# Kernel optimization log

Hardware: AMD Instinct MI355X
Metric: run time of the kernel (lower is better)

## Reference

```python
import jax, jax.numpy as jnp
import numpy as np

B, T, C, H = 2, 2048, 1024, 16
D = C // H  # head dim = 64


def setup_inputs() -> dict:
    key = jax.random.key(0)
    k1, k2, k3 = jax.random.split(key, 3)
    x = jax.random.normal(k1, (B, T, C), dtype=jnp.float32)
    w_attn = jax.random.normal(k2, (C, 3 * C), dtype=jnp.float32) * (1.0 / np.sqrt(C))
    b_attn = jnp.zeros((3 * C,), dtype=jnp.float32)
    w_proj = jax.random.normal(k3, (C, C), dtype=jnp.float32) * (1.0 / np.sqrt(C))
    b_proj = jnp.zeros((C,), dtype=jnp.float32)
    return {"x": x, "w_attn": w_attn, "b_attn": b_attn, "w_proj": w_proj, "b_proj": b_proj}


def reference(x, w_attn, b_attn, w_proj, b_proj):
    Bx, Tx, Cx = x.shape
    qkv = x @ w_attn + b_attn  # [B, T, 3C]
    q, k, v = jnp.split(qkv, 3, axis=-1)
    # [B, H, T, D]
    q = q.reshape(Bx, Tx, H, D).swapaxes(1, 2)
    k = k.reshape(Bx, Tx, H, D).swapaxes(1, 2)
    v = v.reshape(Bx, Tx, H, D).swapaxes(1, 2)
    scale = 1.0 / jnp.sqrt(jnp.float32(D))
    att = jnp.einsum('bhqd,bhkd->bhqk', q, k) * scale  # [B, H, T, T]
    causal = jnp.tril(jnp.ones((Tx, Tx), dtype=bool))
    att = jnp.where(causal[None, None], att, -jnp.inf)
    att = jax.nn.softmax(att, axis=-1)
    y = jnp.einsum('bhqk,bhkd->bhqd', att, v)  # [B, H, T, D]
    y = y.swapaxes(1, 2).reshape(Bx, Tx, Cx)
    return y @ w_proj + b_proj
```

## Files before the change

### kernel.cpp

```cpp
#include <hip/hip_runtime.h>
#include <hip/hip_bf16.h>


typedef __attribute__((ext_vector_type(8))) short short8x;
typedef __attribute__((ext_vector_type(4))) float float4x;
typedef __attribute__((ext_vector_type(4))) unsigned short ushort4x;
typedef __attribute__((ext_vector_type(2))) unsigned int uint2x;

#define MFMA_BF16 __builtin_amdgcn_mfma_f32_16x16x32_bf16

typedef const __attribute__((address_space(1))) void gvoid_t;
typedef __attribute__((address_space(3))) void lvoid_t;
#define GLOAD_LDS16(g, l) __builtin_amdgcn_global_load_lds((gvoid_t*)(g), (lvoid_t*)(l), 16, 0, 0)

__device__ __forceinline__ unsigned short f2b(float f) {
    unsigned int u = __float_as_uint(f);
    u = (u + 0x7FFFu + ((u >> 16) & 1u)) >> 16;
    return (unsigned short)u;
}
__device__ __forceinline__ unsigned int pk2(float a, float b) {
    return __builtin_amdgcn_perm(__float_as_uint(b) + 0x8000u,
                                 __float_as_uint(a) + 0x8000u, 0x07060302u);
}

__device__ __forceinline__ void stage32(const unsigned short* g, size_t rs,
                                        short* ldst, int w0, int lane) {
    const int r8 = lane >> 3;
    const int sc = ((lane & 7) ^ r8) * 8;
#pragma unroll
    for (int q = 0; q < 4; q++) {
        GLOAD_LDS16(g + (size_t)(w0 + q * 8 + r8) * rs + sc,
                    ldst + (w0 + q * 8) * 64);
    }
}

__global__ __launch_bounds__(256) void cast_bf16(const float* __restrict__ in,
                                                 unsigned short* __restrict__ out,
                                                 int n4) {
    int i = blockIdx.x * 256 + threadIdx.x;
    if (i < n4) {
        float4 v = ((const float4*)in)[i];
        ushort4x o = { f2b(v.x), f2b(v.y), f2b(v.z), f2b(v.w) };
        ((ushort4x*)out)[i] = o;
    }
}

__global__ __launch_bounds__(256) void transpose_cast2(const float* __restrict__ wa,
                                                       unsigned short* __restrict__ waT,
                                                       const float* __restrict__ wp,
                                                       unsigned short* __restrict__ wpT) {
    __shared__ float tile[32][33];
    int bx = blockIdx.x;
    const float* in;
    unsigned short* outp;
    int cols;
    if (bx < 96) { in = wa; outp = waT; cols = 3072; }
    else         { in = wp; outp = wpT; cols = 1024; bx -= 96; }
    int cbase = bx * 32;
    int rbase = blockIdx.y * 32;
    int c = cbase + threadIdx.x;
    for (int j = 0; j < 32; j += 8)
        tile[threadIdx.y + j][threadIdx.x] = in[(size_t)(rbase + threadIdx.y + j) * cols + c];
    __syncthreads();
    int rr = rbase + threadIdx.x;
    for (int j = 0; j < 32; j += 8) {
        int cc = cbase + threadIdx.y + j;
        outp[(size_t)cc * 1024 + rr] = f2b(tile[threadIdx.x][threadIdx.y + j]);
    }
}

__global__ __launch_bounds__(256) void gemm_qkv(const unsigned short* __restrict__ A,
                                                const unsigned short* __restrict__ BT,
                                                const float* __restrict__ bias,
                                                unsigned short* __restrict__ QK,
                                                unsigned short* __restrict__ VTg) {
    __shared__ union {
        struct { short A[128 * 64]; short B[128 * 64]; } s;
        short vt[4][64 * 80];
    } lds;

    const int K = 1024;
    const int lane = threadIdx.x & 63;
    const int wave = threadIdx.x >> 6;
    const int quad = lane >> 4;
    const int l16  = lane & 15;
    const int sw   = l16 & 7;

    const int rblk = blockIdx.y * 128;
    const int cblk = blockIdx.x * 128;
    const int wr = wave >> 1, wc = wave & 1;

    float4x acc[4][4] = {};

    const unsigned short* Ag = A  + (size_t)rblk * K;
    const unsigned short* Bg = BT + (size_t)cblk * K;

    for (int kk = 0; kk < K; kk += 64) {
        stage32(Ag + kk, K, lds.s.A, wave * 32, lane);
        stage32(Bg + kk, K, lds.s.B, wave * 32, lane);
        __syncthreads();

#pragma unroll
        for (int kk2 = 0; kk2 < 2; kk2++) {
            short8x a[4], b[4];
#pragma unroll
            for (int i = 0; i < 4; i++)
                a[i] = *(const short8x*)&lds.s.A[(wr * 64 + i * 16 + l16) * 64 +
                                                 ((kk2 * 4 + quad) ^ sw) * 8];
#pragma unroll
            for (int j = 0; j < 4; j++)
                b[j] = *(const short8x*)&lds.s.B[(wc * 64 + j * 16 + l16) * 64 +
                                                 ((kk2 * 4 + quad) ^ sw) * 8];
#pragma unroll
            for (int i = 0; i < 4; i++)
#pragma unroll
                for (int j = 0; j < 4; j++)
                    acc[i][j] = MFMA_BF16(a[i], b[j], acc[i][j], 0, 0, 0);
        }
        __syncthreads();
    }

    const int rbase = rblk + wr * 64;
    const int cbase = cblk + wc * 64;

    if (cbase < 2048) {
        const float QS = 0.18033688f;
#pragma unroll
        for (int i = 0; i < 4; i++) {
#pragma unroll
            for (int j = 0; j < 4; j++) {
                int c = cbase + j * 16 + l16;
                float bv = bias[c];
                float sc = (c < 1024) ? QS : 1.0f;
#pragma unroll
                for (int reg = 0; reg < 4; reg++) {
                    int r = rbase + i * 16 + quad * 4 + reg;
                    QK[(size_t)r * 2048 + c] = f2b((acc[i][j][reg] + bv) * sc);
                }
            }
        }
    } else {
#pragma unroll
        for (int i = 0; i < 4; i++) {
#pragma unroll
            for (int j = 0; j < 4; j++) {
                int c = cbase + j * 16 + l16;
                float bv = bias[c];
                uint2x p = { pk2(acc[i][j][0] + bv, acc[i][j][1] + bv),
                             pk2(acc[i][j][2] + bv, acc[i][j][3] + bv) };
                *(uint2x*)&lds.vt[wave][(j * 16 + l16) * 80 + i * 16 + quad * 4] = p;
            }
        }
        const int h   = (cbase - 2048) >> 6;
        const int hb  = (rbase >> 11) * 16 + h;
        const int tb0 = rbase & 2047;
#pragma unroll
        for (int p = 0; p < 8; p++) {
            int dd   = p * 8 + (lane >> 3);
            int toff = (lane & 7) * 8;
            short8x vv = *(const short8x*)&lds.vt[wave][dd * 80 + toff];
            *(short8x*)&VTg[((size_t)(hb * 64 + dd)) * 2048 + tb0 + toff] = vv;
        }
    }
}

__global__ __launch_bounds__(256) void gemm_proj(const unsigned short* __restrict__ A,
                                                 const unsigned short* __restrict__ BT,
                                                 const float* __restrict__ bias,
                                                 float* __restrict__ out) {
    __shared__ struct { short A[64 * 64]; short B[64 * 64]; } lds;

    const int K = 1024, N = 1024;
    const int lane = threadIdx.x & 63;
    const int wave = threadIdx.x >> 6;
    const int quad = lane >> 4;
    const int l16  = lane & 15;
    const int sw   = l16 & 7;

    const int rblk = blockIdx.y * 64;
    const int cblk = blockIdx.x * 64;

    float4x acc[4] = {};

    const unsigned short* Ag = A  + (size_t)rblk * K;
    const unsigned short* Bg = BT + (size_t)cblk * K;

    for (int kk = 0; kk < K; kk += 64) {
        if (wave < 2) stage32(Ag + kk, K, lds.A, wave * 32, lane);
        else          stage32(Bg + kk, K, lds.B, (wave - 2) * 32, lane);
        __syncthreads();

#pragma unroll
        for (int kk2 = 0; kk2 < 2; kk2++) {
            short8x bfr = *(const short8x*)&lds.B[(wave * 16 + l16) * 64 +
                                                  ((kk2 * 4 + quad) ^ sw) * 8];
#pragma unroll
            for (int i = 0; i < 4; i++) {
                short8x a = *(const short8x*)&lds.A[(i * 16 + l16) * 64 +
                                                    ((kk2 * 4 + quad) ^ sw) * 8];
                acc[i] = MFMA_BF16(a, bfr, acc[i], 0, 0, 0);
            }
        }
        __syncthreads();
    }

    const int c = cblk + wave * 16 + l16;
    const float bv = bias[c];
#pragma unroll
    for (int i = 0; i < 4; i++) {
#pragma unroll
        for (int reg = 0; reg < 4; reg++) {
            int r = rblk + i * 16 + quad * 4 + reg;
            out[(size_t)r * N + c] = acc[i][reg] + bv;
        }
    }
}

__global__ __launch_bounds__(256) void attn_kernel(const unsigned short* __restrict__ QK,
                                                   const unsigned short* __restrict__ VT,
                                                   unsigned short* __restrict__ Y) {
    __shared__ __attribute__((aligned(16))) short Kl[2][64 * 64];
    __shared__ __attribute__((aligned(16))) short Vl[2][64 * 64];
    __shared__ __attribute__((aligned(16))) short Pl[4][16 * 64];

    const int tid  = threadIdx.x;
    const int lane = tid & 63;
    const int wave = tid >> 6;
    const int quad = lane >> 4;
    const int l16  = lane & 15;
    const int sw   = l16 & 7;

    const int bid = blockIdx.x;
    const int v2  = (bid >> 8) & 3;
    const int s2  = ((bid >> 3) & 3) ^ v2;
    const int m3  = (bid >> 5) & 7;
    const int qb  = (s2 == 0) ? m3 : (s2 == 1) ? 15 - m3
                  : (s2 == 2) ? 16 + m3 : 31 - m3;
    const int bh  = (bid & 7) | (v2 << 3);
    const int b = bh >> 4, h = bh & 15;

    const unsigned short* Qp = QK + ((size_t)b * 2048) * 2048 + h * 64;
    const unsigned short* Kp = Qp + 1024;
    const unsigned short* Vp = VT + (size_t)bh * 64 * 2048;

    const int qbase = qb * 64 + wave * 16;
    const int ntb   = qb + 1;

    short8x aq[2];
#pragma unroll
    for (int kk = 0; kk < 2; kk++)
        aq[kk] = *(const short8x*)(Qp + (size_t)(qbase + l16) * 2048 + kk * 32 + quad * 8);

    if (wave < 2) stage32(Kp, 2048, Kl[0], wave * 32, lane);
    else          stage32(Vp, 2048, Vl[0], (wave - 2) * 32, lane);
    __syncthreads();

    float l = 0.f;
    float4x O[4] = {};

    for (int it = 0; it < ntb; it++) {
        const int kb = it * 64;
        const short* Kc = Kl[it & 1];
        const short* Vc = Vl[it & 1];

        if (it + 1 < ntb) {
            const int kb2 = kb + 64;
            if (wave < 2) stage32(Kp + (size_t)kb2 * 2048, 2048, Kl[(it + 1) & 1], wave * 32, lane);
            else          stage32(Vp + kb2, 2048, Vl[(it + 1) & 1], (wave - 2) * 32, lane);
        }

        float4x S[4];
#pragma unroll
        for (int t = 0; t < 4; t++) {
            short8x kf0 = *(const short8x*)&Kc[(t * 16 + l16) * 64 + ((quad) ^ sw) * 8];
            short8x kf1 = *(const short8x*)&Kc[(t * 16 + l16) * 64 + ((4 + quad) ^ sw) * 8];
            S[t] = (float4x){0.f, 0.f, 0.f, 0.f};
            S[t] = MFMA_BF16(kf0, aq[0], S[t], 0, 0, 0);
            S[t] = MFMA_BF16(kf1, aq[1], S[t], 0, 0, 0);
        }

        if (kb + 64 > qbase) {
            int q = qbase + l16;
#pragma unroll
            for (int t = 0; t < 4; t++)
#pragma unroll
                for (int reg = 0; reg < 4; reg++)
                    if (kb + t * 16 + quad * 4 + reg > q) S[t][reg] = -1e38f;
        }

#pragma unroll
        for (int t = 0; t < 4; t++) {
            float e0 = __builtin_amdgcn_exp2f(S[t][0]);
            float e1 = __builtin_amdgcn_exp2f(S[t][1]);
            float e2 = __builtin_amdgcn_exp2f(S[t][2]);
            float e3 = __builtin_amdgcn_exp2f(S[t][3]);
            l += (e0 + e1) + (e2 + e3);
            uint2x p = { pk2(e0, e1), pk2(e2, e3) };
            *(uint2x*)&Pl[wave][l16 * 64 + ((2 * t + (quad >> 1)) ^ sw) * 8 + (quad & 1) * 4] = p;
        }

#pragma unroll
        for (int kc = 0; kc < 2; kc++) {
            short8x bp = *(const short8x*)&Pl[wave][l16 * 64 + ((4 * kc + quad) ^ sw) * 8];
#pragma unroll
            for (int dt = 0; dt < 4; dt++) {
                short8x vf = *(const short8x*)&Vc[(dt * 16 + l16) * 64 + ((kc * 4 + quad) ^ sw) * 8];
                O[dt] = MFMA_BF16(vf, bp, O[dt], 0, 0, 0);
            }
        }
        __syncthreads();
    }

    float lv = l;
    lv += __shfl_xor(lv, 16, 64);
    lv += __shfl_xor(lv, 32, 64);
    float rl = 1.0f / lv;
#pragma unroll
    for (int dt = 0; dt < 4; dt++) {
        uint2x o = { pk2(O[dt][0] * rl, O[dt][1] * rl),
                     pk2(O[dt][2] * rl, O[dt][3] * rl) };
        *(uint2x*)&Pl[wave][l16 * 64 + ((2 * dt + (quad >> 1)) ^ sw) * 8 + (quad & 1) * 4] = o;
    }
    const int t = qbase + l16;
#pragma unroll
    for (int cc = 0; cc < 2; cc++) {
        short8x row = *(const short8x*)&Pl[wave][l16 * 64 + ((2 * quad + cc) ^ sw) * 8];
        *(short8x*)&Y[((size_t)(b * 2048 + t)) * 1024 + h * 64 + (2 * quad + cc) * 8] = row;
    }
}

extern "C" void kernel_launch(void* const* d_in, const int* in_sizes, int n_in,
                              void* d_out, int out_size, void* d_ws, size_t ws_size,
                              hipStream_t stream) {
    const float* x      = (const float*)d_in[0];
    const float* w_attn = (const float*)d_in[1];
    const float* b_attn = (const float*)d_in[2];
    const float* w_proj = (const float*)d_in[3];
    const float* b_proj = (const float*)d_in[4];
    float* out = (float*)d_out;

    char* ws = (char*)d_ws;
    unsigned short* xb  = (unsigned short*)(ws + (size_t)0);
    unsigned short* waT = (unsigned short*)(ws + (size_t)(8  << 20));
    unsigned short* wpT = (unsigned short*)(ws + (size_t)(14 << 20));
    unsigned short* QKb = (unsigned short*)(ws + (size_t)(16 << 20));
    unsigned short* VTb = (unsigned short*)(ws + (size_t)(32 << 20));
    unsigned short* yb  = (unsigned short*)(ws + (size_t)(40 << 20));

    cast_bf16<<<4096, 256, 0, stream>>>(x, xb, 1048576);

    transpose_cast2<<<dim3(128, 32), dim3(32, 8), 0, stream>>>(w_attn, waT, w_proj, wpT);

    gemm_qkv<<<dim3(24, 32), 256, 0, stream>>>(xb, waT, b_attn, QKb, VTb);

    attn_kernel<<<1024, 256, 0, stream>>>(QKb, VTb, yb);

    gemm_proj<<<dim3(16, 64), 256, 0, stream>>>(yb, wpT, b_proj, out);
}
```

Baseline: 182.3 us.

## Double-buffer LDS staging in QKV and projection GEMMs, vectorize Q/K stores

Both GEMMs now prefetch the next K-slice into a second LDS buffer while computing on the current one, so global-to-LDS loads overlap MFMA work. The QKV GEMM moves to 32-wide K tiles with a new swizzle so the doubled buffers fit in the same LDS footprint. For Q/K tiles it swaps the MFMA operands so each lane holds four consecutive columns, which allows packed 8-byte bf16 stores and float4 bias loads. This adds per-iteration branching and changes the synchronisation pattern; the loop tail in the new code is not fully visible.

```diff
diff --git a/kernel.cpp b/kernel.cpp
--- a/kernel.cpp
+++ b/kernel.cpp
@@ -31,6 +31,17 @@
     for (int q = 0; q < 4; q++) {
         GLOAD_LDS16(g + (size_t)(w0 + q * 8 + r8) * rs + sc,
                     ldst + (w0 + q * 8) * 64);
+    }
+}
+
+__device__ __forceinline__ void stage32k32(const unsigned short* g, size_t rs,
+                                           short* ldst, int w0, int lane) {
+    const int r4 = lane >> 2;
+    const int sc = ((lane & 3) ^ ((lane >> 3) & 3)) * 8;
+#pragma unroll
+    for (int q = 0; q < 2; q++) {
+        GLOAD_LDS16(g + (size_t)(w0 + q * 16 + r4) * rs + sc,
+                    ldst + (w0 + q * 16) * 32);
     }
 }
 
@@ -75,7 +86,7 @@
                                                 unsigned short* __restrict__ QK,
                                                 unsigned short* __restrict__ VTg) {
     __shared__ union {
-        struct { short A[128 * 64]; short B[128 * 64]; } s;
+        struct { short A[2][128 * 32]; short B[2][128 * 32]; } s;
         short vt[4][64 * 80];
     } lds;
 
@@ -84,33 +95,43 @@
     const int wave = threadIdx.x >> 6;
     const int quad = lane >> 4;
     const int l16  = lane & 15;
-    const int sw   = l16 & 7;
+    const int co   = (quad ^ ((l16 >> 1) & 3)) * 8;
 
     const int rblk = blockIdx.y * 128;
     const int cblk = blockIdx.x * 128;
     const int wr = wave >> 1, wc = wave & 1;
+    const bool qk = (blockIdx.x < 16);
 
     float4x acc[4][4] = {};
 
     const unsigned short* Ag = A  + (size_t)rblk * K;
     const unsigned short* Bg = BT + (size_t)cblk * K;
 
-    for (int kk = 0; kk < K; kk += 64) {
-        stage32(Ag + kk, K, lds.s.A, wave * 32, lane);
-        stage32(Bg + kk, K, lds.s.B, wave * 32, lane);
-        __syncthreads();
-
-#pragma unroll
-        for (int kk2 = 0; kk2 < 2; kk2++) {
-            short8x a[4], b[4];
+    stage32k32(Ag, K, lds.s.A[0], wave * 32, lane);
+    stage32k32(Bg, K, lds.s.B[0], wave * 32, lane);
+    __syncthreads();
+
+    for (int it = 0; it < 32; ++it) {
+        const short* As = lds.s.A[it & 1];
+        const short* Bs = lds.s.B[it & 1];
+        if (it + 1 < 32) {
+            stage32k32(Ag + (it + 1) * 32, K, lds.s.A[(it + 1) & 1], wave * 32, lane);
+            stage32k32(Bg + (it + 1) * 32, K, lds.s.B[(it + 1) & 1], wave * 32, lane);
+        }
+        short8x a[4], b[4];
+#pragma unroll
+        for (int i = 0; i < 4; i++)
+            a[i] = *(const short8x*)&As[(wr * 64 + i * 16 + l16) * 32 + co];
+#pragma unroll
+        for (int j = 0; j < 4; j++)
+            b[j] = *(const short8x*)&Bs[(wc * 64 + j * 16 + l16) * 32 + co];
+        if (qk) {
 #pragma unroll
             for (int i = 0; i < 4; i++)
-                a[i] = *(const short8x*)&lds.s.A[(wr * 64 + i * 16 + l16) * 64 +
-                                                 ((kk2 * 4 + quad) ^ sw) * 8];
-#pragma unroll
-            for (int j = 0; j < 4; j++)
-                b[j] = *(const short8x*)&lds.s.B[(wc * 64 + j * 16 + l16) * 64 +
-                                                 ((kk2 * 4 + quad) ^ sw) * 8];
+#pragma unroll
+                for (int j = 0; j < 4; j++)
+                    acc[i][j] = MFMA_BF16(b[j], a[i], acc[i][j], 0, 0, 0);
+        } else {
 #pragma unroll
             for (int i = 0; i < 4; i++)
 #pragma unroll
@@ -123,20 +144,18 @@
     const int rbase = rblk + wr * 64;
     const int cbase = cblk + wc * 64;
 
-    if (cbase < 2048) {
-        const float QS = 0.18033688f;
+    if (qk) {
+        const float sc = (blockIdx.x < 8) ? 0.18033688f : 1.0f;
 #pragma unroll
         for (int i = 0; i < 4; i++) {
+            const int r = rbase + i * 16 + l16;
 #pragma unroll
             for (int j = 0; j < 4; j++) {
-                int c = cbase + j * 16 + l16;
-                float bv = bias[c];
-                float sc = (c < 1024) ? QS : 1.0f;
-#pragma unroll
-                for (int reg = 0; reg < 4; reg++) {
-                    int r = rbase + i * 16 + quad * 4 + reg;
-                    QK[(size_t)r * 2048 + c] = f2b((acc[i][j][reg] + bv) * sc);
-                }
+                const int c = cbase + j * 16 + quad * 4;
+                float4 bv = *(const float4*)&bias[c];
+                uint2x p = { pk2((acc[i][j][0] + bv.x) * sc, (acc[i][j][1] + bv.y) * sc),
+                             pk2((acc[i][j][2] + bv.z) * sc, (acc[i][j][3] + bv.w) * sc) };
+                *(uint2x*)&QK[(size_t)r * 2048 + c] = p;
             }
         }
     } else {
@@ -168,7 +187,7 @@
                                                  const unsigned short* __restrict__ BT,
                                                  const float* __restrict__ bias,
                                                  float* __restrict__ out) {
-    __shared__ struct { short A[64 * 64]; short B[64 * 64]; } lds;
+    __shared__ struct { short A[2][64 * 64]; short B[2][64 * 64]; } lds;
 
     const int K = 1024, N = 1024;
     const int lane = threadIdx.x & 63;
@@ -185,19 +204,26 @@
     const unsigned short* Ag = A  + (size_t)rblk * K;
     const unsigned short* Bg = BT + (size_t)cblk * K;
 
-    for (int kk = 0; kk < K; kk += 64) {
-        if (wave < 2) stage32(Ag + kk, K, lds.A, wave * 32, lane);
-        else          stage32(Bg + kk, K, lds.B, (wave - 2) * 32, lane);
-        __syncthreads();
-
+    if (wave < 2) stage32(Ag, K, lds.A[0], wave * 32, lane);
+    else          stage32(Bg, K, lds.B[0], (wave - 2) * 32, lane);
+    __syncthreads();
+
+    for (int it = 0; it < 16; ++it) {
+        const short* As = lds.A[it & 1];
+        const short* Bs = lds.B[it & 1];
+        if (it + 1 < 16) {
+            const int kk = (it + 1) * 64;
+            if (wave < 2) stage32(Ag + kk, K, lds.A[(it + 1) & 1], wave * 32, lane);
+            else          stage32(Bg + kk, K, lds.B[(it + 1) & 1], (wave - 2) * 32, lane);
+        }
 #pragma unroll
         for (int kk2 = 0; kk2 < 2; kk2++) {
-            short8x bfr = *(const short8x*)&lds.B[(wave * 16 + l16) * 64 +
-                                                  ((kk2 * 4 + quad) ^ sw) * 8];
+            short8x bfr = *(const short8x*)&Bs[(wave * 16 + l16) * 64 +
+                                               ((kk2 * 4 + quad) ^ sw) * 8];
 #pragma unroll
             for (int i = 0; i < 4; i++) {
-                short8x a = *(const short8x*)&lds.A[(i * 16 + l16) * 64 +
-                                                    ((kk2 * 4 + quad) ^ sw) * 8];
+                short8x a = *(const short8x*)&As[(i * 16 + l16) * 64 +
+                                                 ((kk2 * 4 + quad) ^ sw) * 8];
                 acc[i] = MFMA_BF16(a, bfr, acc[i], 0, 0, 0);
             }
         }
```

Result: slower. 195.7 us (+7.3%).
